# Performance work log

Hardware: AMD Instinct MI355X
Metric: run time of the kernel (lower is better)

## Reference

```python
import jax, jax.numpy as jnp
import numpy as np

B, T, E = 16, 4096, 768
NEG = -10000000000.0

def setup_inputs() -> dict:
    key = jax.random.key(0)
    k1, k2, k3, k4 = jax.random.split(key, 4)
    query = jax.random.normal(k1, (B, E), dtype=jnp.float32)
    context = jax.random.normal(k2, (B, T, E), dtype=jnp.float32)
    mask = jax.random.randint(k3, (B, T), 0, 2, dtype=jnp.int32)
    # guarantee at least one unmasked position per row
    mask = mask.at[:, 0].set(1)
    v_w = jax.random.normal(k4, (2 * E,), dtype=jnp.float32) * (1.0 / np.sqrt(2 * E))
    return {"query": query, "context": context, "mask": mask, "v_w": v_w}

def reference(query, context, mask, v_w):
    # query: [b,e] -> broadcast to [b,t,e]; cat with context -> [b,t,2e]
    q = jnp.broadcast_to(query[:, None, :], context.shape)
    # score = tanh(cat([q, c])) . v_w ; split dot to avoid materializing concat
    scores = jnp.tanh(q) @ v_w[:context.shape[-1]] + jnp.tanh(context) @ v_w[context.shape[-1]:]  # [b,t]
    scores = jnp.where(mask < 1, NEG, scores)
    attn = jax.nn.softmax(scores, axis=-1)              # [b,t]
    return jnp.einsum("bt,bte->be", attn, context)      # [b,e]
```

## Files before the change

### kernel.cpp

```cpp
#include <hip/hip_runtime.h>

constexpr int Bc = 16;
constexpr int Tc = 4096;
constexpr int Ec = 768;
constexpr int PSTRIDE = Ec + 4;

__device__ __forceinline__ float fast_tanh(float x) {
    x = fminf(12.0f, fmaxf(-12.0f, x));
    float e = __expf(2.0f * x);
    return fmaf(-2.0f, __builtin_amdgcn_rcpf(e + 1.0f), 1.0f);
}

__device__ __forceinline__ float dot_tanh4(float4 c, float4 w) {
    float s = fast_tanh(c.x) * w.x;
    s = fmaf(fast_tanh(c.y), w.y, s);
    s = fmaf(fast_tanh(c.z), w.z, s);
    s = fmaf(fast_tanh(c.w), w.w, s);
    return s;
}

__device__ __forceinline__ float4 ld4(const float* p) {
    return *reinterpret_cast<const float4*>(p);
}

using vf4 = __attribute__((ext_vector_type(4))) float;
__device__ __forceinline__ float4 ldnt4(const float* p) {
    vf4 v = __builtin_nontemporal_load(reinterpret_cast<const vf4*>(p));
    return make_float4(v.x, v.y, v.z, v.w);
}

template<int C>
__global__ __launch_bounds__(256, 4) void attn_partial(
    const float* __restrict__ ctx, const int* __restrict__ mask,
    const float* __restrict__ v_w, float* __restrict__ parts)
{
    constexpr int RPB = Tc / C;
    constexpr int R   = RPB / 4;
    const int b    = blockIdx.x / C;
    const int c    = blockIdx.x % C;
    const int wave = threadIdx.x >> 6;
    const int lane = threadIdx.x & 63;

    const float4 vw0 = ld4(v_w + Ec + 0 * 256 + 4 * lane);
    const float4 vw1 = ld4(v_w + Ec + 1 * 256 + 4 * lane);
    const float4 vw2 = ld4(v_w + Ec + 2 * 256 + 4 * lane);

    float  l  = 0.0f;
    float4 o0 = make_float4(0.f, 0.f, 0.f, 0.f), o1 = o0, o2 = o0;

    const int    row0 = c * RPB + wave * R;
    const float* cb   = ctx + (long)b * Tc * Ec;

    for (int g = 0; g < R; g += 64) {
        const int n  = (R - g < 64) ? (R - g) : 64;
        const int li = (lane < n) ? lane : 0;
        const int mv = mask[b * Tc + row0 + g + li];
        unsigned long long mb = __ballot(lane < n && mv != 0);
        const int cnt = __popcll(mb);
        if (!cnt) continue;

        auto pop = [&]() -> const float* {
            int r = (int)__ffsll((long long)mb) - 1; mb &= mb - 1;
            return cb + (long)(row0 + g + r) * Ec + 4 * lane;
        };

        float4 a0, a1, a2, a3, a4, a5;
        auto compute_pair = [&]() {
            float s0 = dot_tanh4(a0, vw0) + dot_tanh4(a1, vw1) + dot_tanh4(a2, vw2);
            float s1 = dot_tanh4(a3, vw0) + dot_tanh4(a4, vw1) + dot_tanh4(a5, vw2);
#pragma unroll
            for (int off = 32; off > 0; off >>= 1) {
                s0 += __shfl_xor(s0, off, 64);
                s1 += __shfl_xor(s1, off, 64);
            }
            const float p0 = __expf(s0), p1 = __expf(s1);
            l += p0 + p1;
            o0.x = fmaf(p0, a0.x, fmaf(p1, a3.x, o0.x));
            o0.y = fmaf(p0, a0.y, fmaf(p1, a3.y, o0.y));
            o0.z = fmaf(p0, a0.z, fmaf(p1, a3.z, o0.z));
            o0.w = fmaf(p0, a0.w, fmaf(p1, a3.w, o0.w));
            o1.x = fmaf(p0, a1.x, fmaf(p1, a4.x, o1.x));
            o1.y = fmaf(p0, a1.y, fmaf(p1, a4.y, o1.y));
            o1.z = fmaf(p0, a1.z, fmaf(p1, a4.z, o1.z));
            o1.w = fmaf(p0, a1.w, fmaf(p1, a4.w, o1.w));
            o2.x = fmaf(p0, a2.x, fmaf(p1, a5.x, o2.x));
            o2.y = fmaf(p0, a2.y, fmaf(p1, a5.y, o2.y));
            o2.z = fmaf(p0, a2.z, fmaf(p1, a5.z, o2.z));
            o2.w = fmaf(p0, a2.w, fmaf(p1, a5.w, o2.w));
        };

        const int pairs = cnt >> 1;
        if (pairs) {
            { const float* p = pop(); a0 = ldnt4(p); a1 = ldnt4(p + 256); a2 = ldnt4(p + 512);
              const float* q = pop(); a3 = ldnt4(q); a4 = ldnt4(q + 256); a5 = ldnt4(q + 512); }
            for (int pi = 1; pi < pairs; ++pi) {
                const float* p = pop();
                float4 n0 = ldnt4(p), n1 = ldnt4(p + 256), n2 = ldnt4(p + 512);
                const float* q = pop();
                float4 n3 = ldnt4(q), n4 = ldnt4(q + 256), n5 = ldnt4(q + 512);
                compute_pair();
                a0 = n0; a1 = n1; a2 = n2; a3 = n3; a4 = n4; a5 = n5;
            }
            compute_pair();
        }
        if (cnt & 1) {
            const float* p = pop();
            a0 = ldnt4(p); a1 = ldnt4(p + 256); a2 = ldnt4(p + 512);
            float s = dot_tanh4(a0, vw0) + dot_tanh4(a1, vw1) + dot_tanh4(a2, vw2);
#pragma unroll
            for (int off = 32; off > 0; off >>= 1)
                s += __shfl_xor(s, off, 64);
            const float pw = __expf(s);
            l += pw;
            o0.x = fmaf(pw, a0.x, o0.x); o0.y = fmaf(pw, a0.y, o0.y);
            o0.z = fmaf(pw, a0.z, o0.z); o0.w = fmaf(pw, a0.w, o0.w);
            o1.x = fmaf(pw, a1.x, o1.x); o1.y = fmaf(pw, a1.y, o1.y);
            o1.z = fmaf(pw, a1.z, o1.z); o1.w = fmaf(pw, a1.w, o1.w);
            o2.x = fmaf(pw, a2.x, o2.x); o2.y = fmaf(pw, a2.y, o2.y);
            o2.w = fmaf(pw, a2.w, o2.w); o2.z = fmaf(pw, a2.z, o2.z);
        }
    }

    __shared__ float sl[4];
    __shared__ float so[4][Ec];
    if (lane == 0) sl[wave] = l;
    *reinterpret_cast<float4*>(&so[wave][0 * 256 + 4 * lane]) = o0;
    *reinterpret_cast<float4*>(&so[wave][1 * 256 + 4 * lane]) = o1;
    *reinterpret_cast<float4*>(&so[wave][2 * 256 + 4 * lane]) = o2;
    __syncthreads();

    float* part = parts + ((long)b * C + c) * PSTRIDE;
    if (threadIdx.x == 0) part[0] = sl[0] + sl[1] + sl[2] + sl[3];
    if (threadIdx.x < 192) {
        const int e = 4 * threadIdx.x;
        float4 s0 = *reinterpret_cast<float4*>(&so[0][e]);
        float4 s1 = *reinterpret_cast<float4*>(&so[1][e]);
        float4 s2 = *reinterpret_cast<float4*>(&so[2][e]);
        float4 s3 = *reinterpret_cast<float4*>(&so[3][e]);
        float4 rs = make_float4(s0.x + s1.x + s2.x + s3.x,
                                s0.y + s1.y + s2.y + s3.y,
                                s0.z + s1.z + s2.z + s3.z,
                                s0.w + s1.w + s2.w + s3.w);
        *reinterpret_cast<float4*>(part + 4 + e) = rs;
    }
}

template<int C>
__global__ __launch_bounds__(256) void attn_reduce(
    const float* __restrict__ parts, float* __restrict__ out)
{
    const int b   = blockIdx.x;
    const int tid = threadIdx.x;
    const float* pb = parts + (long)b * C * PSTRIDE;

    float lsum = 0.0f;
#pragma unroll
    for (int k = 0; k < C; ++k) lsum += pb[k * PSTRIDE];

    const int e = blockIdx.y * 256 + tid;
    float acc = 0.0f;
#pragma unroll
    for (int k = 0; k < C; ++k) acc += pb[k * PSTRIDE + 4 + e];

    out[b * Ec + e] = acc / lsum;
}

template<int C>
static void run_pipeline(const float* ctx, const int* mask, const float* vw,
                         float* ws, float* out, hipStream_t stream)
{
    attn_partial<C><<<dim3(Bc * C), 256, 0, stream>>>(ctx, mask, vw, ws);
    attn_reduce<C><<<dim3(Bc, 3), 256, 0, stream>>>(ws, out);
}

extern "C" void kernel_launch(void* const* d_in, const int* in_sizes, int n_in,
                              void* d_out, int out_size, void* d_ws, size_t ws_size,
                              hipStream_t stream)
{
    (void)in_sizes; (void)n_in; (void)out_size;
    const float* ctx  = (const float*)d_in[1];
    const int*   mask = (const int*)d_in[2];
    const float* vw   = (const float*)d_in[3];
    float* out = (float*)d_out;
    float* ws  = (float*)d_ws;

    const size_t need32 = (size_t)Bc * 32 * PSTRIDE * sizeof(float);
    const size_t need8  = (size_t)Bc * 8  * PSTRIDE * sizeof(float);
    const size_t need2  = (size_t)Bc * 2  * PSTRIDE * sizeof(float);

    if (ws_size >= need32)     run_pipeline<32>(ctx, mask, vw, ws, out, stream);
    else if (ws_size >= need8) run_pipeline<8>(ctx, mask, vw, ws, out, stream);
    else if (ws_size >= need2) run_pipeline<2>(ctx, mask, vw, ws, out, stream);
    else                       run_pipeline<1>(ctx, mask, vw, ws, out, stream);
}
```

Before: 249.9 us.

## Interleave unmasked rows across waves and double the chunk count

Each block's four waves now share one 64-row mask group and split its unmasked rows round-robin, instead of each wave taking its own contiguous range. This balances work between waves when the mask density varies locally. The per-batch chunk count doubles (64/16/4), giving more blocks, at the cost of more partials to reduce. The tanh input clamp is also dropped to save two ALU ops per element, which relies on __expf overflow still producing a correct saturated result.

```diff
diff --git a/kernel.cpp b/kernel.cpp
--- a/kernel.cpp
+++ b/kernel.cpp
@@ -6,7 +6,6 @@
 constexpr int PSTRIDE = Ec + 4;
 
 __device__ __forceinline__ float fast_tanh(float x) {
-    x = fminf(12.0f, fmaxf(-12.0f, x));
     float e = __expf(2.0f * x);
     return fmaf(-2.0f, __builtin_amdgcn_rcpf(e + 1.0f), 1.0f);
 }
@@ -35,7 +34,6 @@
     const float* __restrict__ v_w, float* __restrict__ parts)
 {
     constexpr int RPB = Tc / C;
-    constexpr int R   = RPB / 4;
     const int b    = blockIdx.x / C;
     const int c    = blockIdx.x % C;
     const int wave = threadIdx.x >> 6;
@@ -48,20 +46,23 @@
     float  l  = 0.0f;
     float4 o0 = make_float4(0.f, 0.f, 0.f, 0.f), o1 = o0, o2 = o0;
 
-    const int    row0 = c * RPB + wave * R;
-    const float* cb   = ctx + (long)b * Tc * Ec;
+    const int    brow0 = c * RPB;
+    const float* cb    = ctx + (long)b * Tc * Ec;
 
-    for (int g = 0; g < R; g += 64) {
-        const int n  = (R - g < 64) ? (R - g) : 64;
-        const int li = (lane < n) ? lane : 0;
-        const int mv = mask[b * Tc + row0 + g + li];
-        unsigned long long mb = __ballot(lane < n && mv != 0);
+    for (int g = 0; g < RPB; g += 64) {
+        const int mv = mask[b * Tc + brow0 + g + lane];
+        unsigned long long mb = __ballot(mv != 0);
         const int cnt = __popcll(mb);
-        if (!cnt) continue;
+        mb &= mb - (wave >= 1);
+        mb &= mb - (wave >= 2);
+        mb &= mb - (wave >= 3);
+        const int mycnt = (cnt > wave) ? ((cnt - wave + 3) >> 2) : 0;
+        if (!mycnt) continue;
 
         auto pop = [&]() -> const float* {
-            int r = (int)__ffsll((long long)mb) - 1; mb &= mb - 1;
-            return cb + (long)(row0 + g + r) * Ec + 4 * lane;
+            int r = (int)__ffsll((long long)mb) - 1;
+            mb &= mb - 1; mb &= mb - 1; mb &= mb - 1; mb &= mb - 1;
+            return cb + (long)(brow0 + g + r) * Ec + 4 * lane;
         };
 
         float4 a0, a1, a2, a3, a4, a5;
@@ -89,7 +90,7 @@
             o2.w = fmaf(p0, a2.w, fmaf(p1, a5.w, o2.w));
         };
 
-        const int pairs = cnt >> 1;
+        const int pairs = mycnt >> 1;
         if (pairs) {
             { const float* p = pop(); a0 = ldnt4(p); a1 = ldnt4(p + 256); a2 = ldnt4(p + 512);
               const float* q = pop(); a3 = ldnt4(q); a4 = ldnt4(q + 256); a5 = ldnt4(q + 512); }
@@ -103,7 +104,7 @@
             }
             compute_pair();
         }
-        if (cnt & 1) {
+        if (mycnt & 1) {
             const float* p = pop();
             a0 = ldnt4(p); a1 = ldnt4(p + 256); a2 = ldnt4(p + 512);
             float s = dot_tanh4(a0, vw0) + dot_tanh4(a1, vw1) + dot_tanh4(a2, vw2);
@@ -117,7 +118,7 @@
             o1.x = fmaf(pw, a1.x, o1.x); o1.y = fmaf(pw, a1.y, o1.y);
             o1.z = fmaf(pw, a1.z, o1.z); o1.w = fmaf(pw, a1.w, o1.w);
             o2.x = fmaf(pw, a2.x, o2.x); o2.y = fmaf(pw, a2.y, o2.y);
-            o2.w = fmaf(pw, a2.w, o2.w); o2.z = fmaf(pw, a2.z, o2.z);
+            o2.z = fmaf(pw, a2.z, o2.z); o2.w = fmaf(pw, a2.w, o2.w);
         }
     }
 
@@ -184,12 +185,12 @@
     float* out = (float*)d_out;
     float* ws  = (float*)d_ws;
 
-    const size_t need32 = (size_t)Bc * 32 * PSTRIDE * sizeof(float);
-    const size_t need8  = (size_t)Bc * 8  * PSTRIDE * sizeof(float);
-    const size_t need2  = (size_t)Bc * 2  * PSTRIDE * sizeof(float);
+    const size_t need64 = (size_t)Bc * 64 * PSTRIDE * sizeof(float);
+    const size_t need16 = (size_t)Bc * 16 * PSTRIDE * sizeof(float);
+    const size_t need4  = (size_t)Bc * 4  * PSTRIDE * sizeof(float);
 
-    if (ws_size >= need32)     run_pipeline<32>(ctx, mask, vw, ws, out, stream);
-    else if (ws_size >= need8) run_pipeline<8>(ctx, mask, vw, ws, out, stream);
-    else if (ws_size >= need2) run_pipeline<2>(ctx, mask, vw, ws, out, stream);
-    else                       run_pipeline<1>(ctx, mask, vw, ws, out, stream);
+    if (ws_size >= need64)      run_pipeline<64>(ctx, mask, vw, ws, out, stream);
+    else if (ws_size >= need16) run_pipeline<16>(ctx, mask, vw, ws, out, stream);
+    else if (ws_size >= need4)  run_pipeline<4>(ctx, mask, vw, ws, out, stream);
+    else                        run_pipeline<1>(ctx, mask, vw, ws, out, stream);
 }
```

Measured after the change: 250.8 us. Within noise of the previous version (+0.4%).
